# Optimization experiments

Hardware: AMD Instinct MI355X
Metric: run time of the kernel (lower is better)

## Reference

```python
import jax, jax.numpy as jnp
import numpy as np

HIDDEN = 2048
NUM_HEADS = 16
NUM_KV_HEADS = 4
HEAD_DIM = HIDDEN // NUM_HEADS  # 128
GROUPS = NUM_HEADS // NUM_KV_HEADS  # 4
ROPE_DIMS = 32
QK_GAIN = 6.0
B, T = 2, 2048


def _rope_cos_sin(T, dtype):
    pos = jnp.arange(T, dtype=jnp.float32)
    inv_freq = 1.0 / (10000.0 ** (jnp.arange(0, ROPE_DIMS, 2, dtype=jnp.float32) / ROPE_DIMS))
    freqs = jnp.outer(pos, inv_freq)                  # [T, ROPE/2]
    freqs = jnp.concatenate([freqs, freqs], axis=-1)  # [T, ROPE]
    return jnp.cos(freqs).astype(dtype), jnp.sin(freqs).astype(dtype)


def _apply_rope(t, cos_f, sin_f):
    # t: [B, H, T, head_dim]; rope on first ROPE_DIMS, pass-through on the rest
    t_rt, t_pass = t[..., :ROPE_DIMS], t[..., ROPE_DIMS:]
    h1, h2 = jnp.split(t_rt, 2, axis=-1)
    rot = jnp.concatenate([-h2, h1], axis=-1)
    return jnp.concatenate([t_rt * cos_f + rot * sin_f, t_pass], axis=-1)


def setup_inputs() -> dict:
    key = jax.random.key(0)
    ks = jax.random.split(key, 5)
    s = 0.02
    return {
        "x": jax.random.normal(ks[0], (B, T, HIDDEN), jnp.float32),
        "Wq": jax.random.normal(ks[1], (HIDDEN, HIDDEN), jnp.float32) * s,
        "Wk": jax.random.normal(ks[2], (HIDDEN, NUM_KV_HEADS * HEAD_DIM), jnp.float32) * s,
        "Wv": jax.random.normal(ks[3], (HIDDEN, NUM_KV_HEADS * HEAD_DIM), jnp.float32) * s,
        "Wo": jax.random.normal(ks[4], (HIDDEN, HIDDEN), jnp.float32) * s,
    }


def reference(x, Wq, Wk, Wv, Wo):
    Bx, Tx, C = x.shape
    q = (x @ Wq).reshape(Bx, Tx, NUM_HEADS, HEAD_DIM).transpose(0, 2, 1, 3)      # [B,H,T,d]
    k = (x @ Wk).reshape(Bx, Tx, NUM_KV_HEADS, HEAD_DIM).transpose(0, 2, 1, 3)   # [B,KV,T,d]
    v = (x @ Wv).reshape(Bx, Tx, NUM_KV_HEADS, HEAD_DIM).transpose(0, 2, 1, 3)   # [B,KV,T,d]

    cos_f, sin_f = _rope_cos_sin(Tx, q.dtype)  # [T, ROPE]
    q = _apply_rope(q, cos_f, sin_f)
    k = _apply_rope(k, cos_f, sin_f)

    # GQA: group query heads per kv head instead of repeat_interleave-ing K/V
    qg = q.reshape(Bx, NUM_KV_HEADS, GROUPS, Tx, HEAD_DIM)
    scale = QK_GAIN / jnp.sqrt(jnp.asarray(HEAD_DIM, q.dtype))
    scores = jnp.einsum('bkgqd,bkld->bkgql', qg * scale, k)  # [B,KV,G,T,T]
    causal = jnp.tril(jnp.ones((Tx, Tx), dtype=bool))
    scores = jnp.where(causal, scores, jnp.asarray(-jnp.inf, scores.dtype))
    probs = jax.nn.softmax(scores, axis=-1)
    out = jnp.einsum('bkgql,bkld->bkgqd', probs, v)          # [B,KV,G,T,d]
    out = out.reshape(Bx, NUM_HEADS, Tx, HEAD_DIM).transpose(0, 2, 1, 3).reshape(Bx, Tx, C)
    return out @ Wo
```

## Files before the change

kernel.cpp:

```cpp
#include <hip/hip_runtime.h>
#include <hip/hip_bf16.h>
#include <cstdint>
#include <cstddef>

typedef unsigned short u16;
typedef short s16x8 __attribute__((ext_vector_type(8)));
typedef float f32x4 __attribute__((ext_vector_type(4)));
typedef u16 u16x4 __attribute__((ext_vector_type(4)));

#define HIDDEN_C 2048
#define TSEQ 2048
#define BATCH 2
#define NHEADS 16
#define NKV 4
#define HDIM 128
#define NQKV 3072
#define BTR 4096

__device__ __forceinline__ float bf2f(u16 u) {
  union { uint32_t i; float f; } v; v.i = ((uint32_t)u) << 16; return v.f;
}
__device__ __forceinline__ u16 f2bf(float f) {
  union { float f; uint32_t i; } v; v.f = f;
  uint32_t r = v.i + 0x7fffu + ((v.i >> 16) & 1u);
  return (u16)(r >> 16);
}

#define AS1(p) ((__attribute__((address_space(1))) void*)(uintptr_t)(p))
#define AS3(p) ((__attribute__((address_space(3))) void*)(p))

__global__ void convert_x_kernel(const float* __restrict__ x, u16* __restrict__ xb) {
  int i = (blockIdx.x * blockDim.x + threadIdx.x) * 8;
  float4 a = *(const float4*)(x + i);
  float4 b = *(const float4*)(x + i + 4);
  uint4 o;
  o.x = (uint32_t)f2bf(a.x) | ((uint32_t)f2bf(a.y) << 16);
  o.y = (uint32_t)f2bf(a.z) | ((uint32_t)f2bf(a.w) << 16);
  o.z = (uint32_t)f2bf(b.x) | ((uint32_t)f2bf(b.y) << 16);
  o.w = (uint32_t)f2bf(b.z) | ((uint32_t)f2bf(b.w) << 16);
  *(uint4*)(xb + i) = o;
}

__global__ void transpose_w_kernel(const float* __restrict__ in, u16* __restrict__ out,
                                   int R, int C) {
  __shared__ float tile[32][33];
  int r0 = blockIdx.y * 32, c0 = blockIdx.x * 32;
  int tx = threadIdx.x, ty = threadIdx.y;
  #pragma unroll
  for (int i = 0; i < 32; i += 8)
    tile[ty + i][tx] = in[(size_t)(r0 + ty + i) * C + c0 + tx];
  __syncthreads();
  #pragma unroll
  for (int i = 0; i < 32; i += 8)
    out[(size_t)(c0 + ty + i) * R + r0 + tx] = f2bf(tile[tx][ty + i]);
}

template <typename OutT>
__global__ __launch_bounds__(256) void gemm_bt_kernel(const u16* __restrict__ A,
                                                      const u16* __restrict__ BT,
                                                      OutT* __restrict__ C,
                                                      int M, int N, int K) {
  __shared__ u16 As[128 * 32];
  __shared__ u16 Bs[128 * 32];
  const int tid = threadIdx.x;
  const int wave = tid >> 6, lane = tid & 63;
  const int lr = lane & 15, lg = lane >> 4;
  const int m0 = blockIdx.y * 128, n0 = blockIdx.x * 128;
  const int wr = wave >> 1, wc = wave & 1;
  f32x4 acc[4][4];
  #pragma unroll
  for (int a = 0; a < 4; ++a)
    #pragma unroll
    for (int b = 0; b < 4; ++b) acc[a][b] = (f32x4){0.f, 0.f, 0.f, 0.f};

  for (int k0 = 0; k0 < K; k0 += 32) {
    #pragma unroll
    for (int i = 0; i < 2; ++i) {
      int c = tid + i * 256;
      int row = c >> 2, col8 = (c & 3) * 8;
      const u16* gA = A + (size_t)(m0 + row) * K + k0 + col8;
      const u16* gB = BT + (size_t)(n0 + row) * K + k0 + col8;
      char* lA = (char*)As + ((size_t)(wave * 64 + i * 256)) * 16;
      char* lB = (char*)Bs + ((size_t)(wave * 64 + i * 256)) * 16;
      __builtin_amdgcn_global_load_lds(AS1(gA), AS3(lA), 16, 0, 0);
      __builtin_amdgcn_global_load_lds(AS1(gB), AS3(lB), 16, 0, 0);
    }
    __syncthreads();
    s16x8 af[4], bfr[4];
    #pragma unroll
    for (int mi = 0; mi < 4; ++mi)
      af[mi] = *(const s16x8*)(As + (wr * 64 + mi * 16 + lr) * 32 + lg * 8);
    #pragma unroll
    for (int ni = 0; ni < 4; ++ni)
      bfr[ni] = *(const s16x8*)(Bs + (wc * 64 + ni * 16 + lr) * 32 + lg * 8);
    #pragma unroll
    for (int mi = 0; mi < 4; ++mi)
      #pragma unroll
      for (int ni = 0; ni < 4; ++ni)
        acc[mi][ni] = __builtin_amdgcn_mfma_f32_16x16x32_bf16(af[mi], bfr[ni], acc[mi][ni], 0, 0, 0);
    __syncthreads();
  }
  #pragma unroll
  for (int mi = 0; mi < 4; ++mi) {
    int rowb = m0 + wr * 64 + mi * 16 + lg * 4;
    #pragma unroll
    for (int ni = 0; ni < 4; ++ni) {
      int col = n0 + wc * 64 + ni * 16 + lr;
      #pragma unroll
      for (int r = 0; r < 4; ++r) {
        float v = acc[mi][ni][r];
        if constexpr (sizeof(OutT) == 2) C[(size_t)(rowb + r) * N + col] = (OutT)f2bf(v);
        else                             C[(size_t)(rowb + r) * N + col] = v;
      }
    }
  }
}

__global__ void rope_kernel(u16* __restrict__ base, int col_off, int head_shift, float scale) {
  int idx = blockIdx.x * blockDim.x + threadIdx.x;
  int quarter = idx & 3;
  int hidx = idx >> 2;
  int head = hidx & ((1 << head_shift) - 1);
  int bt = hidx >> head_shift;
  if (bt >= BTR) return;
  int t = bt & (TSEQ - 1);
  u16* p = base + (size_t)bt * NQKV + col_off + head * HDIM + quarter * 32;
  uint4 u[4];
  #pragma unroll
  for (int j = 0; j < 4; ++j) u[j] = ((const uint4*)p)[j];
  float v[32];
  #pragma unroll
  for (int j = 0; j < 4; ++j) {
    v[j*8+0] = bf2f((u16)(u[j].x & 0xffff)); v[j*8+1] = bf2f((u16)(u[j].x >> 16));
    v[j*8+2] = bf2f((u16)(u[j].y & 0xffff)); v[j*8+3] = bf2f((u16)(u[j].y >> 16));
    v[j*8+4] = bf2f((u16)(u[j].z & 0xffff)); v[j*8+5] = bf2f((u16)(u[j].z >> 16));
    v[j*8+6] = bf2f((u16)(u[j].w & 0xffff)); v[j*8+7] = bf2f((u16)(u[j].w >> 16));
  }
  if (quarter == 0) {
    #pragma unroll
    for (int i = 0; i < 16; ++i) {
      float f = powf(10000.f, -(float)i * (1.f / 16.f));
      float ang = (float)t * f;
      float s = sinf(ang), c = cosf(ang);
      float a = v[i], b = v[i + 16];
      v[i]      = a * c - b * s;
      v[i + 16] = b * c + a * s;
    }
  }
  #pragma unroll
  for (int i = 0; i < 32; ++i) v[i] *= scale;
  #pragma unroll
  for (int j = 0; j < 4; ++j) {
    u[j].x = (uint32_t)f2bf(v[j*8+0]) | ((uint32_t)f2bf(v[j*8+1]) << 16);
    u[j].y = (uint32_t)f2bf(v[j*8+2]) | ((uint32_t)f2bf(v[j*8+3]) << 16);
    u[j].z = (uint32_t)f2bf(v[j*8+4]) | ((uint32_t)f2bf(v[j*8+5]) << 16);
    u[j].w = (uint32_t)f2bf(v[j*8+6]) | ((uint32_t)f2bf(v[j*8+7]) << 16);
  }
  #pragma unroll
  for (int j = 0; j < 4; ++j) ((uint4*)p)[j] = u[j];
}

__global__ void transpose_v_kernel(const u16* __restrict__ qkv, u16* __restrict__ vt) {
  int bg = blockIdx.z;
  int b = bg >> 2, g = bg & 3;
  int t0 = blockIdx.x * 32, d0 = blockIdx.y * 32;
  __shared__ u16 tile[32][33];
  int tx = threadIdx.x, ty = threadIdx.y;
  #pragma unroll
  for (int i = 0; i < 32; i += 8)
    tile[ty + i][tx] = qkv[(size_t)(b * TSEQ + t0 + ty + i) * NQKV + 2560 + g * HDIM + d0 + tx];
  __syncthreads();
  #pragma unroll
  for (int i = 0; i < 32; i += 8)
    vt[((size_t)bg * HDIM + d0 + ty + i) * TSEQ + t0 + tx] = tile[tx][ty + i];
}

__global__ __launch_bounds__(256, 2) void attn_kernel(const u16* __restrict__ qkv,
                                                      const u16* __restrict__ vt,
                                                      u16* __restrict__ attn_out) {
  __shared__ u16 K_lds[2][64][128];
  __shared__ u16 V_lds[2][128][64];
  __shared__ u16 P_lds[4][2][16][64];

  const int idx = blockIdx.x;
  const int h = idx & 15, b = (idx >> 4) & 1, g = h >> 2;
  const int j = (idx >> 5) & 7;
  const int tile = (idx >> 8) ? j : 15 - j;
  const int tid = threadIdx.x, w = tid >> 6, lane = tid & 63;
  const int lr = lane & 15, lg = lane >> 4;
  const int q0 = tile * 128;
  const int q0w = q0 + w * 32;
  const int swz = (lr & 7) << 3;

  const u16* Qg = qkv + (size_t)b * TSEQ * NQKV + h * HDIM;
  const u16* Kg = qkv + (size_t)b * TSEQ * NQKV + HIDDEN_C + g * HDIM;
  const u16* Vg = vt + (size_t)(b * NKV + g) * HDIM * TSEQ;

  s16x8 aq[2][4];
  #pragma unroll
  for (int mi = 0; mi < 2; ++mi) {
    const u16* qrow = Qg + (size_t)(q0w + mi * 16 + lr) * NQKV + lg * 8;
    #pragma unroll
    for (int kk = 0; kk < 4; ++kk) aq[mi][kk] = *(const s16x8*)(qrow + kk * 32);
  }

  f32x4 O[2][8];
  #pragma unroll
  for (int mi = 0; mi < 2; ++mi)
    #pragma unroll
    for (int dt = 0; dt < 8; ++dt) O[mi][dt] = (f32x4){0.f, 0.f, 0.f, 0.f};
  float m_r[2] = {-1e30f, -1e30f}, l_r[2] = {0.f, 0.f};

  auto STAGE = [&](int buf, int kb) {
    #pragma unroll
    for (int i = 0; i < 4; ++i) {
      int c = tid + i * 256;
      int row = c >> 4, slot = c & 15;
      int gslot = slot ^ (row & 7);
      const u16* src = Kg + (size_t)(kb + row) * NQKV + gslot * 8;
      char* dst = (char*)&K_lds[buf][0][0] + (size_t)c * 16;
      __builtin_amdgcn_global_load_lds(AS1(src), AS3(dst), 16, 0, 0);
    }
    #pragma unroll
    for (int i = 0; i < 4; ++i) {
      int c = tid + i * 256;
      int row = c >> 3, slot = c & 7;
      int gslot = slot ^ (row & 7);
      const u16* src = Vg + (size_t)row * TSEQ + kb + gslot * 8;
      char* dst = (char*)&V_lds[buf][0][0] + (size_t)c * 16;
      __builtin_amdgcn_global_load_lds(AS1(src), AS3(dst), 16, 0, 0);
    }
  };

  const int nt = (q0 + 128) / 64;
  STAGE(0, 0);
  asm volatile("s_waitcnt vmcnt(0)" ::: "memory");
  __syncthreads();

  for (int t = 0; t < nt; ++t) {
    const int kb = t * 64;
    const int cur = t & 1;
    if (t + 1 < nt) STAGE(cur ^ 1, kb + 64);

    if (kb <= q0w + 31) {
      f32x4 S[2][4];
      #pragma unroll
      for (int mi = 0; mi < 2; ++mi)
        #pragma unroll
        for (int ni = 0; ni < 4; ++ni) S[mi][ni] = (f32x4){0.f, 0.f, 0.f, 0.f};
      __builtin_amdgcn_s_setprio(1);
      #pragma unroll
      for (int ni = 0; ni < 4; ++ni) {
        const u16* krow = &K_lds[cur][ni * 16 + lr][0];
        #pragma unroll
        for (int kk = 0; kk < 4; ++kk) {
          s16x8 bk = *(const s16x8*)(krow + ((kk * 32 + lg * 8) ^ swz));
          #pragma unroll
          for (int mi = 0; mi < 2; ++mi)
            S[mi][ni] = __builtin_amdgcn_mfma_f32_16x16x32_bf16(bk, aq[mi][kk], S[mi][ni], 0, 0, 0);
        }
      }
      __builtin_amdgcn_s_setprio(0);
      if (kb + 63 > q0w) {
        #pragma unroll
        for (int mi = 0; mi < 2; ++mi) {
          int qrow = q0w + mi * 16 + lr;
          #pragma unroll
          for (int ni = 0; ni < 4; ++ni) {
            int kbase = kb + ni * 16 + lg * 4;
            #pragma unroll
            for (int r = 0; r < 4; ++r)
              if (kbase + r > qrow) S[mi][ni][r] = -1e30f;
          }
        }
      }
      #pragma unroll
      for (int mi = 0; mi < 2; ++mi) {
        f32x4 mm01, mm;
        #pragma unroll
        for (int r = 0; r < 4; ++r) mm01[r] = fmaxf(S[mi][0][r], S[mi][1][r]);
        #pragma unroll
        for (int r = 0; r < 4; ++r) mm[r] = fmaxf(mm01[r], fmaxf(S[mi][2][r], S[mi][3][r]));
        float v = fmaxf(fmaxf(mm[0], mm[1]), fmaxf(mm[2], mm[3]));
        v = fmaxf(v, __shfl_xor(v, 16));
        v = fmaxf(v, __shfl_xor(v, 32));
        float mn = fmaxf(m_r[mi], v);
        float al = __expf(m_r[mi] - mn);
        m_r[mi] = mn;
        f32x4 psv = (f32x4){0.f, 0.f, 0.f, 0.f};
        #pragma unroll
        for (int ni = 0; ni < 4; ++ni)
          #pragma unroll
          for (int r = 0; r < 4; ++r) {
            float p = __expf(S[mi][ni][r] - mn);
            S[mi][ni][r] = p;
            psv[r] += p;
          }
        float ps = (psv[0] + psv[1]) + (psv[2] + psv[3]);
        ps += __shfl_xor(ps, 16);
        ps += __shfl_xor(ps, 32);
        l_r[mi] = l_r[mi] * al + ps;
        #pragma unroll
        for (int dt = 0; dt < 8; ++dt)
          #pragma unroll
          for (int r = 0; r < 4; ++r) O[mi][dt][r] *= al;
        u16* pw = &P_lds[w][mi][lr][0];
        #pragma unroll
        for (int ni = 0; ni < 4; ++ni) {
          u16x4 hq;
          #pragma unroll
          for (int r = 0; r < 4; ++r) hq[r] = f2bf(S[mi][ni][r]);
          *(u16x4*)(pw + ((ni * 16 + lg * 4) ^ swz)) = hq;
        }
      }
      asm volatile("s_waitcnt lgkmcnt(0)" ::: "memory");
      __builtin_amdgcn_sched_barrier(0);
      s16x8 pa[2][2];
      #pragma unroll
      for (int mi = 0; mi < 2; ++mi) {
        const u16* prow = &P_lds[w][mi][lr][0];
        #pragma unroll
        for (int ks = 0; ks < 2; ++ks)
          pa[mi][ks] = *(const s16x8*)(prow + ((ks * 32 + lg * 8) ^ swz));
      }
      __builtin_amdgcn_s_setprio(1);
      #pragma unroll
      for (int dt = 0; dt < 8; ++dt) {
        const u16* vrow = &V_lds[cur][dt * 16 + lr][0];
        #pragma unroll
        for (int ks = 0; ks < 2; ++ks) {
          s16x8 bv = *(const s16x8*)(vrow + ((ks * 32 + lg * 8) ^ swz));
          #pragma unroll
          for (int mi = 0; mi < 2; ++mi)
            O[mi][dt] = __builtin_amdgcn_mfma_f32_16x16x32_bf16(bv, pa[mi][ks], O[mi][dt], 0, 0, 0);
        }
      }
      __builtin_amdgcn_s_setprio(0);
    }
    asm volatile("s_waitcnt vmcnt(0)" ::: "memory");
    __syncthreads();
  }

  #pragma unroll
  for (int mi = 0; mi < 2; ++mi) {
    float invl = 1.f / l_r[mi];
    u16* orow = attn_out + (size_t)(b * TSEQ + q0w + mi * 16 + lr) * HIDDEN_C + h * HDIM + lg * 4;
    #pragma unroll
    for (int dt = 0; dt < 8; ++dt) {
      u16x4 o4;
      #pragma unroll
      for (int r = 0; r < 4; ++r) o4[r] = f2bf(O[mi][dt][r] * invl);
      *(u16x4*)(orow + dt * 16) = o4;
    }
  }
}

extern "C" void kernel_launch(void* const* d_in, const int* in_sizes, int n_in,
                              void* d_out, int out_size, void* d_ws, size_t ws_size,
                              hipStream_t stream) {
  const float* x  = (const float*)d_in[0];
  const float* Wq = (const float*)d_in[1];
  const float* Wk = (const float*)d_in[2];
  const float* Wv = (const float*)d_in[3];
  const float* Wo = (const float*)d_in[4];
  float* out = (float*)d_out;
  char* ws = (char*)d_ws;

  u16* xb    = (u16*)(ws);
  u16* wqkvT = (u16*)(ws + (size_t)(16u << 20));
  u16* woT   = (u16*)(ws + (size_t)(28u << 20));
  u16* qkv   = (u16*)(ws + (size_t)(36u << 20));
  u16* vtb   = (u16*)(ws + (size_t)(60u << 20));
  u16* attn  = (u16*)(ws + (size_t)(64u << 20));

  dim3 tb(32, 8);
  convert_x_kernel<<<(BTR * HIDDEN_C / 8) / 256, 256, 0, stream>>>(x, xb);
  transpose_w_kernel<<<dim3(HIDDEN_C / 32, HIDDEN_C / 32), tb, 0, stream>>>(Wq, wqkvT, HIDDEN_C, HIDDEN_C);
  transpose_w_kernel<<<dim3(512 / 32, HIDDEN_C / 32), tb, 0, stream>>>(Wk, wqkvT + (size_t)2048 * 2048, HIDDEN_C, 512);
  transpose_w_kernel<<<dim3(512 / 32, HIDDEN_C / 32), tb, 0, stream>>>(Wv, wqkvT + (size_t)2560 * 2048, HIDDEN_C, 512);
  transpose_w_kernel<<<dim3(HIDDEN_C / 32, HIDDEN_C / 32), tb, 0, stream>>>(Wo, woT, HIDDEN_C, HIDDEN_C);

  gemm_bt_kernel<u16><<<dim3(NQKV / 128, BTR / 128), 256, 0, stream>>>(xb, wqkvT, qkv, BTR, NQKV, HIDDEN_C);

  const float scale = 0.53033008588991f;
  rope_kernel<<<(BTR * NHEADS * 4) / 256, 256, 0, stream>>>(qkv, 0, 4, scale);
  rope_kernel<<<(BTR * NKV * 4) / 256, 256, 0, stream>>>(qkv, HIDDEN_C, 2, 1.0f);

  transpose_v_kernel<<<dim3(TSEQ / 32, HDIM / 32, BATCH * NKV), tb, 0, stream>>>(qkv, vtb);

  attn_kernel<<<512, 256, 0, stream>>>(qkv, vtb, attn);

  gemm_bt_kernel<float><<<dim3(HIDDEN_C / 128, BTR / 128), 256, 0, stream>>>(attn, woT, out, BTR, HIDDEN_C, HIDDEN_C);
}
```

Measured before the change: 247.7 us.

## Switch attention MFMAs from 16x16x32 to 32x32x16 tiles

Rewrites the attention inner loops to use 32x32x16 bf16 MFMA instructions, with one 32-row Q tile per wave in place of two 16-row tiles. The fragment layouts for Q, K, V, P and O, the causal mask indexing, the softmax row reductions and the P LDS swizzle are all reworked to match. The goal is fewer LDS fragment loads per FLOP and fewer cross-lane shuffles in the softmax. The risk is register pressure from the 16-wide accumulators and possible LDS bank conflicts in the new P layout.

```diff
diff --git a/kernel.cpp b/kernel.cpp
--- a/kernel.cpp
+++ b/kernel.cpp
@@ -6,6 +6,7 @@
 typedef unsigned short u16;
 typedef short s16x8 __attribute__((ext_vector_type(8)));
 typedef float f32x4 __attribute__((ext_vector_type(4)));
+typedef float f32x16 __attribute__((ext_vector_type(16)));
 typedef u16 u16x4 __attribute__((ext_vector_type(4)));
 
 #define HIDDEN_C 2048
@@ -180,36 +181,37 @@
                                                       u16* __restrict__ attn_out) {
   __shared__ u16 K_lds[2][64][128];
   __shared__ u16 V_lds[2][128][64];
-  __shared__ u16 P_lds[4][2][16][64];
+  __shared__ u16 P_lds[4][32][64];
 
   const int idx = blockIdx.x;
   const int h = idx & 15, b = (idx >> 4) & 1, g = h >> 2;
-  const int j = (idx >> 5) & 7;
-  const int tile = (idx >> 8) ? j : 15 - j;
+  const int jb = (idx >> 5) & 7;
+  const int tile = (idx >> 8) ? jb : 15 - jb;
   const int tid = threadIdx.x, w = tid >> 6, lane = tid & 63;
-  const int lr = lane & 15, lg = lane >> 4;
+  const int lq = lane & 31;
+  const int hf = lane >> 5;
   const int q0 = tile * 128;
   const int q0w = q0 + w * 32;
-  const int swz = (lr & 7) << 3;
+  const int swz = (lane & 7) << 3;
+  const int pswz = lq & 7;
 
   const u16* Qg = qkv + (size_t)b * TSEQ * NQKV + h * HDIM;
   const u16* Kg = qkv + (size_t)b * TSEQ * NQKV + HIDDEN_C + g * HDIM;
   const u16* Vg = vt + (size_t)(b * NKV + g) * HDIM * TSEQ;
 
-  s16x8 aq[2][4];
-  #pragma unroll
-  for (int mi = 0; mi < 2; ++mi) {
-    const u16* qrow = Qg + (size_t)(q0w + mi * 16 + lr) * NQKV + lg * 8;
-    #pragma unroll
-    for (int kk = 0; kk < 4; ++kk) aq[mi][kk] = *(const s16x8*)(qrow + kk * 32);
-  }
-
-  f32x4 O[2][8];
-  #pragma unroll
-  for (int mi = 0; mi < 2; ++mi)
-    #pragma unroll
-    for (int dt = 0; dt < 8; ++dt) O[mi][dt] = (f32x4){0.f, 0.f, 0.f, 0.f};
-  float m_r[2] = {-1e30f, -1e30f}, l_r[2] = {0.f, 0.f};
+  s16x8 aq[8];
+  {
+    const u16* qrow = Qg + (size_t)(q0w + lq) * NQKV + hf * 8;
+    #pragma unroll
+    for (int ds = 0; ds < 8; ++ds) aq[ds] = *(const s16x8*)(qrow + ds * 16);
+  }
+
+  f32x16 O[4];
+  #pragma unroll
+  for (int dt = 0; dt < 4; ++dt)
+    #pragma unroll
+    for (int r = 0; r < 16; ++r) O[dt][r] = 0.f;
+  float m_r = -1e30f, l_r = 0.f;
 
   auto STAGE = [&](int buf, int kb) {
     #pragma unroll
@@ -243,96 +245,88 @@
     if (t + 1 < nt) STAGE(cur ^ 1, kb + 64);
 
     if (kb <= q0w + 31) {
-      f32x4 S[2][4];
-      #pragma unroll
-      for (int mi = 0; mi < 2; ++mi)
-        #pragma unroll
-        for (int ni = 0; ni < 4; ++ni) S[mi][ni] = (f32x4){0.f, 0.f, 0.f, 0.f};
+      f32x16 S[2];
+      #pragma unroll
+      for (int kh = 0; kh < 2; ++kh)
+        #pragma unroll
+        for (int r = 0; r < 16; ++r) S[kh][r] = 0.f;
       __builtin_amdgcn_s_setprio(1);
       #pragma unroll
-      for (int ni = 0; ni < 4; ++ni) {
-        const u16* krow = &K_lds[cur][ni * 16 + lr][0];
-        #pragma unroll
-        for (int kk = 0; kk < 4; ++kk) {
-          s16x8 bk = *(const s16x8*)(krow + ((kk * 32 + lg * 8) ^ swz));
-          #pragma unroll
-          for (int mi = 0; mi < 2; ++mi)
-            S[mi][ni] = __builtin_amdgcn_mfma_f32_16x16x32_bf16(bk, aq[mi][kk], S[mi][ni], 0, 0, 0);
+      for (int kh = 0; kh < 2; ++kh) {
+        const u16* krow = &K_lds[cur][kh * 32 + lq][0];
+        #pragma unroll
+        for (int ds = 0; ds < 8; ++ds) {
+          s16x8 ak = *(const s16x8*)(krow + ((ds * 16 + hf * 8) ^ swz));
+          S[kh] = __builtin_amdgcn_mfma_f32_32x32x16_bf16(ak, aq[ds], S[kh], 0, 0, 0);
         }
       }
       __builtin_amdgcn_s_setprio(0);
       if (kb + 63 > q0w) {
-        #pragma unroll
-        for (int mi = 0; mi < 2; ++mi) {
-          int qrow = q0w + mi * 16 + lr;
+        const int q = q0w + lq;
+        #pragma unroll
+        for (int kh = 0; kh < 2; ++kh)
           #pragma unroll
-          for (int ni = 0; ni < 4; ++ni) {
-            int kbase = kb + ni * 16 + lg * 4;
-            #pragma unroll
-            for (int r = 0; r < 4; ++r)
-              if (kbase + r > qrow) S[mi][ni][r] = -1e30f;
+          for (int r = 0; r < 16; ++r) {
+            int k = kb + kh * 32 + (r & 3) + 8 * (r >> 2) + 4 * hf;
+            if (k > q) S[kh][r] = -1e30f;
           }
-        }
-      }
-      #pragma unroll
-      for (int mi = 0; mi < 2; ++mi) {
-        f32x4 mm01, mm;
-        #pragma unroll
-        for (int r = 0; r < 4; ++r) mm01[r] = fmaxf(S[mi][0][r], S[mi][1][r]);
-        #pragma unroll
-        for (int r = 0; r < 4; ++r) mm[r] = fmaxf(mm01[r], fmaxf(S[mi][2][r], S[mi][3][r]));
-        float v = fmaxf(fmaxf(mm[0], mm[1]), fmaxf(mm[2], mm[3]));
-        v = fmaxf(v, __shfl_xor(v, 16));
-        v = fmaxf(v, __shfl_xor(v, 32));
-        float mn = fmaxf(m_r[mi], v);
-        float al = __expf(m_r[mi] - mn);
-        m_r[mi] = mn;
-        f32x4 psv = (f32x4){0.f, 0.f, 0.f, 0.f};
-        #pragma unroll
-        for (int ni = 0; ni < 4; ++ni)
-          #pragma unroll
-          for (int r = 0; r < 4; ++r) {
-            float p = __expf(S[mi][ni][r] - mn);
-            S[mi][ni][r] = p;
-            psv[r] += p;
-          }
-        float ps = (psv[0] + psv[1]) + (psv[2] + psv[3]);
-        ps += __shfl_xor(ps, 16);
-        ps += __shfl_xor(ps, 32);
-        l_r[mi] = l_r[mi] * al + ps;
-        #pragma unroll
-        for (int dt = 0; dt < 8; ++dt)
-          #pragma unroll
-          for (int r = 0; r < 4; ++r) O[mi][dt][r] *= al;
-        u16* pw = &P_lds[w][mi][lr][0];
-        #pragma unroll
-        for (int ni = 0; ni < 4; ++ni) {
+      }
+      f32x16 pm;
+      #pragma unroll
+      for (int r = 0; r < 16; ++r) pm[r] = fmaxf(S[0][r], S[1][r]);
+      float m8[8];
+      #pragma unroll
+      for (int r = 0; r < 8; ++r) m8[r] = fmaxf(pm[r], pm[r + 8]);
+      float mx = fmaxf(fmaxf(fmaxf(m8[0], m8[4]), fmaxf(m8[1], m8[5])),
+                       fmaxf(fmaxf(m8[2], m8[6]), fmaxf(m8[3], m8[7])));
+      mx = fmaxf(mx, __shfl_xor(mx, 32));
+      const float mn = fmaxf(m_r, mx);
+      const float al = __expf(m_r - mn);
+      m_r = mn;
+      #pragma unroll
+      for (int kh = 0; kh < 2; ++kh)
+        #pragma unroll
+        for (int r = 0; r < 16; ++r) S[kh][r] = __expf(S[kh][r] - mn);
+      f32x16 sv;
+      #pragma unroll
+      for (int r = 0; r < 16; ++r) sv[r] = S[0][r] + S[1][r];
+      float s8[8];
+      #pragma unroll
+      for (int r = 0; r < 8; ++r) s8[r] = sv[r] + sv[r + 8];
+      float ps = ((s8[0] + s8[4]) + (s8[1] + s8[5])) + ((s8[2] + s8[6]) + (s8[3] + s8[7]));
+      ps += __shfl_xor(ps, 32);
+      l_r = l_r * al + ps;
+      #pragma unroll
+      for (int dt = 0; dt < 4; ++dt)
+        #pragma unroll
+        for (int r = 0; r < 16; ++r) O[dt][r] *= al;
+      u16* pw = &P_lds[w][lq][0];
+      #pragma unroll
+      for (int kh = 0; kh < 2; ++kh)
+        #pragma unroll
+        for (int r2 = 0; r2 < 4; ++r2) {
           u16x4 hq;
           #pragma unroll
-          for (int r = 0; r < 4; ++r) hq[r] = f2bf(S[mi][ni][r]);
-          *(u16x4*)(pw + ((ni * 16 + lg * 4) ^ swz)) = hq;
+          for (int j = 0; j < 4; ++j) hq[j] = f2bf(S[kh][r2 * 4 + j]);
+          int slot = kh * 4 + r2;
+          *(u16x4*)(pw + ((slot ^ pswz) << 3) + hf * 4) = hq;
         }
-      }
       asm volatile("s_waitcnt lgkmcnt(0)" ::: "memory");
       __builtin_amdgcn_sched_barrier(0);
-      s16x8 pa[2][2];
-      #pragma unroll
-      for (int mi = 0; mi < 2; ++mi) {
-        const u16* prow = &P_lds[w][mi][lr][0];
-        #pragma unroll
-        for (int ks = 0; ks < 2; ++ks)
-          pa[mi][ks] = *(const s16x8*)(prow + ((ks * 32 + lg * 8) ^ swz));
+      s16x8 pb[4];
+      #pragma unroll
+      for (int ks = 0; ks < 4; ++ks) {
+        int slot = ks * 2 + hf;
+        pb[ks] = *(const s16x8*)(pw + ((slot ^ pswz) << 3));
       }
       __builtin_amdgcn_s_setprio(1);
       #pragma unroll
-      for (int dt = 0; dt < 8; ++dt) {
-        const u16* vrow = &V_lds[cur][dt * 16 + lr][0];
-        #pragma unroll
-        for (int ks = 0; ks < 2; ++ks) {
-          s16x8 bv = *(const s16x8*)(vrow + ((ks * 32 + lg * 8) ^ swz));
-          #pragma unroll
-          for (int mi = 0; mi < 2; ++mi)
-            O[mi][dt] = __builtin_amdgcn_mfma_f32_16x16x32_bf16(bv, pa[mi][ks], O[mi][dt], 0, 0, 0);
+      for (int dt = 0; dt < 4; ++dt) {
+        const u16* vrow = &V_lds[cur][dt * 32 + lq][0];
+        #pragma unroll
+        for (int ks = 0; ks < 4; ++ks) {
+          s16x8 av = *(const s16x8*)(vrow + ((ks * 16 + hf * 8) ^ swz));
+          O[dt] = __builtin_amdgcn_mfma_f32_32x32x16_bf16(av, pb[ks], O[dt], 0, 0, 0);
         }
       }
       __builtin_amdgcn_s_setprio(0);
@@ -341,18 +335,17 @@
     __syncthreads();
   }
 
-  #pragma unroll
-  for (int mi = 0; mi < 2; ++mi) {
-    float invl = 1.f / l_r[mi];
-    u16* orow = attn_out + (size_t)(b * TSEQ + q0w + mi * 16 + lr) * HIDDEN_C + h * HDIM + lg * 4;
-    #pragma unroll
-    for (int dt = 0; dt < 8; ++dt) {
+  const float invl = 1.f / l_r;
+  u16* orow = attn_out + (size_t)(b * TSEQ + q0w + lq) * HIDDEN_C + h * HDIM + hf * 4;
+  #pragma unroll
+  for (int dt = 0; dt < 4; ++dt)
+    #pragma unroll
+    for (int r2 = 0; r2 < 4; ++r2) {
       u16x4 o4;
       #pragma unroll
-      for (int r = 0; r < 4; ++r) o4[r] = f2bf(O[mi][dt][r] * invl);
-      *(u16x4*)(orow + dt * 16) = o4;
-    }
-  }
+      for (int j = 0; j < 4; ++j) o4[j] = f2bf(O[dt][r2 * 4 + j] * invl);
+      *(u16x4*)(orow + dt * 32 + r2 * 8) = o4;
+    }
 }
 
 extern "C" void kernel_launch(void* const* d_in, const int* in_sizes, int n_in,
```

Result: no change. 246.4 us (-0.5%).
